# Performance work log

Measured on AMD Instinct MI355X. Metric: run time of the kernel, lower is better.

Reference implementation:

```python
import jax, jax.numpy as jnp
import numpy as np

B, S, D, H = 2, 2048, 1024, 16
HD = D // H  # head_dim = 64


def setup_inputs() -> dict:
    rng = jax.random.key(0)
    ks = jax.random.split(rng, 14)
    s = 0.02
    return {
        "query": jax.random.normal(ks[0], (B, S, D), jnp.float32),
        "key": jax.random.normal(ks[1], (B, S, D), jnp.float32),
        "value": jax.random.normal(ks[2], (B, S, D), jnp.float32),
        "Wq": jax.random.normal(ks[3], (D, D), jnp.float32) * s,
        "bq": jnp.zeros((D,), jnp.float32),
        "Wk": jax.random.normal(ks[4], (D, D), jnp.float32) * s,
        "bk": jnp.zeros((D,), jnp.float32),
        "Wv": jax.random.normal(ks[5], (D, D), jnp.float32) * s,
        "bv": jnp.zeros((D,), jnp.float32),
        "Wo": jax.random.normal(ks[6], (D, D), jnp.float32) * s,
        "bo": jnp.zeros((D,), jnp.float32),
        "Wa": jax.random.normal(ks[7], (3, D, D), jnp.float32) * s,  # 3 aspect projections
        "ba": jnp.zeros((3, D), jnp.float32),
    }


def reference(query, key, value, Wq, bq, Wk, bk, Wv, bv, Wo, bo, Wa, ba):
    scale = 1.0 / jnp.sqrt(jnp.asarray(HD, query.dtype))
    # projections; split heads -> [B, H, S, HD]
    q = (query @ Wq + bq).reshape(B, S, H, HD).transpose(0, 2, 1, 3)
    k = (key @ Wk + bk).reshape(B, S, H, HD).transpose(0, 2, 1, 3)
    v = (value @ Wv + bv).reshape(B, S, H, HD).transpose(0, 2, 1, 3)
    # main attention (dropout p=0, no masks)
    logits = jnp.einsum('bhqd,bhkd->bhqk', q, k) * scale
    attn_weights = jax.nn.softmax(logits, axis=-1)  # [B, H, S, S]
    ctx = jnp.einsum('bhqk,bhkd->bhqd', attn_weights, v)
    attn_output = ctx.transpose(0, 2, 1, 3).reshape(B, S, D) @ Wo + bo
    # 3 interpretable aspect patterns: each proj applied to query and key,
    # full-dim QK^T scaled by sqrt(head_dim), softmax over keys.
    q_asp = jnp.einsum('bsd,ade->abse', query, Wa) + ba[:, None, None, :]
    k_asp = jnp.einsum('bsd,ade->abse', key, Wa) + ba[:, None, None, :]
    pat_logits = jnp.einsum('abqd,abkd->abqk', q_asp, k_asp) * scale
    patterns = jax.nn.softmax(pat_logits, axis=-1)  # [3, B, S, S]
    return attn_output, attn_weights, patterns
```

## Files before the change

kernel.cpp:

```cpp
#include <hip/hip_runtime.h>

typedef unsigned short u16;
typedef short s16x4 __attribute__((ext_vector_type(4)));
typedef short s16x8 __attribute__((ext_vector_type(8)));
typedef float f32x4 __attribute__((ext_vector_type(4)));

#define DEVFN __device__ __forceinline__

constexpr long AW_OFF  = 4194304;
constexpr long PAT_OFF = AW_OFF + 134217728;

DEVFN u16 f2bf(float x) {
  unsigned u = __builtin_bit_cast(unsigned, x);
  unsigned r = (u + 0x7fffu + ((u >> 16) & 1u)) >> 16;
  return (u16)r;
}

DEVFN void gld16(const u16* g, u16* l) {
  __builtin_amdgcn_global_load_lds(
      (const __attribute__((address_space(1))) unsigned int*)g,
      (__attribute__((address_space(3))) unsigned int*)l, 16, 0, 0);
}

__global__ __launch_bounds__(256) void k_cvt3(const float* __restrict__ a,
                                              const float* __restrict__ b,
                                              const float* __restrict__ c,
                                              u16* __restrict__ out, int n4) {
  int i = blockIdx.x * 256 + threadIdx.x;
  if (i >= n4) return;
  const float* in = (blockIdx.y == 0) ? a : (blockIdx.y == 1) ? b : c;
  float4 v = ((const float4*)in)[i];
  s16x4 o; o[0] = f2bf(v.x); o[1] = f2bf(v.y); o[2] = f2bf(v.z); o[3] = f2bf(v.w);
  ((s16x4*)(out + (long)blockIdx.y * 4194304))[i] = o;
}

__global__ __launch_bounds__(256) void k_pack3(const float* __restrict__ a,
                                               const float* __restrict__ b,
                                               const float* __restrict__ c,
                                               float* __restrict__ out) {
  int i = blockIdx.x * 256 + threadIdx.x;
  const float* in = (i < 1024) ? a : (i < 2048) ? b : c;
  out[i] = in[i & 1023];
}

template <bool IN_F32>
__global__ __launch_bounds__(256) void k_tr(const void* __restrict__ inv,
                                            u16* __restrict__ out,
                                            long ldin, long ldout,
                                            long inz1, long inz2, long outz, int zdiv) {
  __shared__ u16 tile[32][33];
  int z = blockIdx.z;
  long ioff = (long)(z / zdiv) * inz1 + (long)(z % zdiv) * inz2;
  int k0 = blockIdx.y * 32, n0 = blockIdx.x * 32;
  int tx = threadIdx.x, ty = threadIdx.y;
#pragma unroll
  for (int i = 0; i < 4; ++i) {
    long k = k0 + ty + i * 8, n = n0 + tx;
    u16 v;
    if constexpr (IN_F32) v = f2bf(((const float*)inv)[ioff + k * ldin + n]);
    else                  v = ((const u16*)inv)[ioff + k * ldin + n];
    tile[ty + i * 8][tx] = v;
  }
  __syncthreads();
  long ooff = (long)z * outz;
#pragma unroll
  for (int i = 0; i < 4; ++i) {
    long n = n0 + ty + i * 8, k = k0 + tx;
    out[ooff + n * ldout + k] = tile[tx][ty + i * 8];
  }
}

template <typename OutT, int EPI>
__global__ __launch_bounds__(256) void k_gemm_nt(
    const u16* __restrict__ Ap, const u16* __restrict__ Bp, OutT* __restrict__ Cp,
    const float* __restrict__ bias, const float* __restrict__ rinv, float alpha, int K,
    long lda, long ldb, long ldc,
    long saz1, long saz2, long sbz1, long sbz2, long scz1, long scz2,
    long sbias, int zdiv) {
  __shared__ __align__(16) u16 At[128][64];
  __shared__ __align__(16) u16 Bt[128][64];
  const int tid = threadIdx.x, lane = tid & 63, wid = tid >> 6;
  const int wm = wid >> 1, wn = wid & 1;

  const int gx = gridDim.x, gy = gridDim.y;
  int id = (blockIdx.z * gy + blockIdx.y) * gx + blockIdx.x;
  const int nb = gx * gy * (int)gridDim.z;
  if ((nb & 7) == 0) id = (id & 7) * (nb >> 3) + (id >> 3);
  const int bxi = id % gx, byi = (id / gx) % gy, bzi = id / (gx * gy);

  const int z = bzi, z1 = z / zdiv, z2 = z % zdiv;
  const u16* Ab = Ap + (long)z1 * saz1 + (long)z2 * saz2;
  const u16* Bb = Bp + (long)z1 * sbz1 + (long)z2 * sbz2;
  OutT* C = Cp + (long)z1 * scz1 + (long)z2 * scz2;
  const float* bv = bias ? bias + (long)z2 * sbias : nullptr;
  const int row0 = byi * 128, col0 = bxi * 128;
  const int lk = lane & 15, g = lane >> 4;

  f32x4 acc[4][4] = {};

  for (int k0 = 0; k0 < K; k0 += 64) {
#pragma unroll
    for (int it = 0; it < 4; ++it) {
      const int u = it * 256 + tid;
      const int r = u >> 3, p = u & 7;
      const int cg = (p ^ (r & 7)) * 8;
      gld16(Ab + (long)(row0 + r) * lda + (k0 + cg), &At[r][p * 8]);
      gld16(Bb + (long)(col0 + r) * ldb + (k0 + cg), &Bt[r][p * 8]);
    }
    __syncthreads();
#pragma unroll
    for (int kk = 0; kk < 2; ++kk) {
      s16x8 af[4], bf[4];
#pragma unroll
      for (int m = 0; m < 4; ++m)
        af[m] = *(const s16x8*)&At[wm * 64 + m * 16 + lk][((kk * 4 + g) ^ (lk & 7)) * 8];
#pragma unroll
      for (int n = 0; n < 4; ++n)
        bf[n] = *(const s16x8*)&Bt[wn * 64 + n * 16 + lk][((kk * 4 + g) ^ (lk & 7)) * 8];
#pragma unroll
      for (int m = 0; m < 4; ++m)
#pragma unroll
        for (int n = 0; n < 4; ++n)
          acc[m][n] = __builtin_amdgcn_mfma_f32_16x16x32_bf16(af[m], bf[n], acc[m][n], 0, 0, 0);
    }
    __syncthreads();
  }

  const float* rz = (EPI == 1) ? rinv + (long)z * 2048 : nullptr;
#pragma unroll
  for (int m = 0; m < 4; ++m) {
    const int grow = row0 + wm * 64 + m * 16 + g * 4;
#pragma unroll
    for (int r = 0; r < 4; ++r) {
      float iv = 0.0f;
      if constexpr (EPI == 1) iv = rz[grow + r];
#pragma unroll
      for (int n = 0; n < 4; ++n) {
        const int gcol = col0 + wn * 64 + n * 16 + lk;
        float v;
        if constexpr (EPI == 1) v = __expf(alpha * acc[m][n][r]) * iv;
        else                    v = alpha * acc[m][n][r] + (bv ? bv[gcol] : 0.0f);
        if constexpr (sizeof(OutT) == 2) C[(long)(grow + r) * ldc + gcol] = f2bf(v);
        else                             C[(long)(grow + r) * ldc + gcol] = v;
      }
    }
  }
}

__global__ __launch_bounds__(256) void k_flash(
    const u16* __restrict__ qp, const u16* __restrict__ kp, const u16* __restrict__ vt,
    u16* __restrict__ ctx, float* __restrict__ rinv) {
  __shared__ __align__(16) char lds[49152];
  u16* Qt = (u16*)lds;
  u16* Kt = (u16*)(lds + 16384);
  u16* Vl = (u16*)(lds + 32768);
  const int tid = threadIdx.x, lane = tid & 63, wid = tid >> 6;
  const int wk = wid >> 1, wq = wid & 1;

  const int gx = gridDim.x;
  int id = blockIdx.y * gx + blockIdx.x;
  const int nb = gx * (int)gridDim.y;
  if ((nb & 7) == 0) id = (id & 7) * (nb >> 3) + (id >> 3);
  const int bh = id / gx, q0 = (id % gx) * 128;

  const long qkbase = (long)(bh >> 4) * 2097152 + (long)(bh & 15) * 64;
  const long vbase = (long)bh * 131072;
  const int lk = lane & 15, g = lane >> 4;
  const int sp = lane & 7;
  const int sr = lane >> 3;

#pragma unroll
  for (int i = 0; i < 4; ++i) {
    const int rr = (wid * 4 + i) * 8 + sr;
    gld16(qp + qkbase + (long)(q0 + rr) * 1024 + ((sp ^ (rr & 7)) * 8), Qt + rr * 64 + sp * 8);
  }
  __syncthreads();

  s16x8 qf[2][4];
#pragma unroll
  for (int kk = 0; kk < 2; ++kk) {
#pragma unroll
    for (int nq = 0; nq < 4; ++nq)
      qf[kk][nq] = *(const s16x8*)(Qt + (wq * 64 + nq * 16 + lk) * 64 + ((kk * 4 + g) ^ (lk & 7)) * 8);
  }

  f32x4 cacc[4][4] = {};
  float rs[4] = {0.f, 0.f, 0.f, 0.f};

  for (int t = 0; t < 16; ++t) {
    const int kb = t * 128;
#pragma unroll
    for (int i = 0; i < 4; ++i) {
      const int rr = (wid * 4 + i) * 8 + sr;
      gld16(kp + qkbase + (long)(kb + rr) * 1024 + ((sp ^ (rr & 7)) * 8), Kt + rr * 64 + sp * 8);
      const int dd = (wid * 4 + i) * 4 + g;
      const int pv = lane & 15;
      const int cv = (pv & 8) | ((pv ^ dd) & 7);
      gld16(vt + vbase + (long)dd * 2048 + (kb + cv * 8), Vl + dd * 128 + pv * 8);
    }
    __syncthreads();

    f32x4 st[4][4] = {};
#pragma unroll
    for (int kk = 0; kk < 2; ++kk) {
      s16x8 af[4];
#pragma unroll
      for (int mk = 0; mk < 4; ++mk)
        af[mk] = *(const s16x8*)(Kt + (wk * 64 + mk * 16 + lk) * 64 + ((kk * 4 + g) ^ (lk & 7)) * 8);
#pragma unroll
      for (int mk = 0; mk < 4; ++mk)
#pragma unroll
        for (int nq = 0; nq < 4; ++nq)
          st[mk][nq] = __builtin_amdgcn_mfma_f32_16x16x32_bf16(af[mk], qf[kk][nq], st[mk][nq], 0, 0, 0);
    }
#pragma unroll
    for (int mk = 0; mk < 4; ++mk)
#pragma unroll
      for (int nq = 0; nq < 4; ++nq)
#pragma unroll
        for (int j = 0; j < 4; ++j) {
          const float p = __expf(st[mk][nq][j] * 0.125f);
          st[mk][nq][j] = p;
          rs[nq] += p;
        }
#pragma unroll
    for (int ks = 0; ks < 2; ++ks) {
      s16x8 pb[4];
#pragma unroll
      for (int nq = 0; nq < 4; ++nq) {
        s16x8 b;
#pragma unroll
        for (int j = 0; j < 4; ++j) {
          b[j]     = (short)f2bf(st[2 * ks][nq][j]);
          b[4 + j] = (short)f2bf(st[2 * ks + 1][nq][j]);
        }
        pb[nq] = b;
      }
#pragma unroll
      for (int md = 0; md < 4; ++md) {
        const int rowv = md * 16 + lk;
        const int u0 = ks * 4 + (g >> 1);
        const int p0 = wk * 8 + ((u0 ^ (rowv & 7)) & 7);
        const int p2 = wk * 8 + (((u0 + 2) ^ (rowv & 7)) & 7);
        const u16* vb0 = Vl + rowv * 128 + p0 * 8 + (g & 1) * 4;
        const u16* vb2 = Vl + rowv * 128 + p2 * 8 + (g & 1) * 4;
        s16x4 lo = *(const s16x4*)vb0;
        s16x4 hi = *(const s16x4*)vb2;
        s16x8 vf;
        vf[0] = lo[0]; vf[1] = lo[1]; vf[2] = lo[2]; vf[3] = lo[3];
        vf[4] = hi[0]; vf[5] = hi[1]; vf[6] = hi[2]; vf[7] = hi[3];
#pragma unroll
        for (int nq = 0; nq < 4; ++nq)
          cacc[md][nq] = __builtin_amdgcn_mfma_f32_16x16x32_bf16(vf, pb[nq], cacc[md][nq], 0, 0, 0);
      }
    }
    __syncthreads();
  }

#pragma unroll
  for (int nq = 0; nq < 4; ++nq) {
    rs[nq] += __shfl_xor(rs[nq], 16, 64);
    rs[nq] += __shfl_xor(rs[nq], 32, 64);
  }
  float* ctxl = (float*)lds;
  float* rsl  = (float*)(lds + 33024);
  if (wk == 1) {
#pragma unroll
    for (int md = 0; md < 4; ++md)
#pragma unroll
      for (int nq = 0; nq < 4; ++nq)
#pragma unroll
        for (int r = 0; r < 4; ++r)
          ctxl[(md * 16 + g * 4 + r) * 129 + wq * 64 + nq * 16 + lk] = cacc[md][nq][r];
    if (lane < 16)
#pragma unroll
      for (int nq = 0; nq < 4; ++nq) rsl[wq * 64 + nq * 16 + lane] = rs[nq];
  }
  __syncthreads();
  if (wk == 0) {
#pragma unroll
    for (int md = 0; md < 4; ++md)
#pragma unroll
      for (int nq = 0; nq < 4; ++nq)
#pragma unroll
        for (int r = 0; r < 4; ++r) {
          const int idx = (md * 16 + g * 4 + r) * 129 + wq * 64 + nq * 16 + lk;
          ctxl[idx] += cacc[md][nq][r];
        }
    if (lane < 16)
#pragma unroll
      for (int nq = 0; nq < 4; ++nq) {
        const int qi = wq * 64 + nq * 16 + lane;
        const float inv = 1.0f / (rsl[qi] + rs[nq]);
        rsl[qi] = inv;
        rinv[(long)bh * 2048 + q0 + qi] = inv;
      }
  }
  __syncthreads();
  const int qr = tid >> 1, half = tid & 1;
  const float inv = rsl[qr];
  u16* dst = ctx + (long)(bh >> 4) * 2097152 + (long)(q0 + qr) * 1024 + (long)(bh & 15) * 64 + half * 32;
#pragma unroll
  for (int c = 0; c < 4; ++c) {
    s16x8 o;
#pragma unroll
    for (int j = 0; j < 8; ++j) {
      const int d = half * 32 + c * 8 + j;
      o[j] = (short)f2bf(ctxl[d * 129 + qr] * inv);
    }
    ((s16x8*)dst)[c] = o;
  }
}

__global__ __launch_bounds__(256) void k_softmax(float* __restrict__ base) {
  float* p = base + (long)blockIdx.x * 2048;
  const int t = threadIdx.x;
  float4 v0 = ((const float4*)p)[t];
  float4 v1 = ((const float4*)p)[t + 256];
  float m = fmaxf(fmaxf(fmaxf(v0.x, v0.y), fmaxf(v0.z, v0.w)),
                  fmaxf(fmaxf(v1.x, v1.y), fmaxf(v1.z, v1.w)));
#pragma unroll
  for (int i = 32; i >= 1; i >>= 1) m = fmaxf(m, __shfl_xor(m, i, 64));
  __shared__ float sm[4], ss[4];
  if ((t & 63) == 0) sm[t >> 6] = m;
  __syncthreads();
  m = fmaxf(fmaxf(sm[0], sm[1]), fmaxf(sm[2], sm[3]));
  float4 e0, e1;
  e0.x = __expf(v0.x - m); e0.y = __expf(v0.y - m); e0.z = __expf(v0.z - m); e0.w = __expf(v0.w - m);
  e1.x = __expf(v1.x - m); e1.y = __expf(v1.y - m); e1.z = __expf(v1.z - m); e1.w = __expf(v1.w - m);
  float s = (e0.x + e0.y + e0.z + e0.w) + (e1.x + e1.y + e1.z + e1.w);
#pragma unroll
  for (int i = 32; i >= 1; i >>= 1) s += __shfl_xor(s, i, 64);
  if ((t & 63) == 0) ss[t >> 6] = s;
  __syncthreads();
  s = ss[0] + ss[1] + ss[2] + ss[3];
  float inv = 1.0f / s;
  e0.x *= inv; e0.y *= inv; e0.z *= inv; e0.w *= inv;
  e1.x *= inv; e1.y *= inv; e1.z *= inv; e1.w *= inv;
  ((float4*)p)[t] = e0;
  ((float4*)p)[t + 256] = e1;
}

extern "C" void kernel_launch(void* const* d_in, const int* in_sizes, int n_in,
                              void* d_out, int out_size, void* d_ws, size_t ws_size,
                              hipStream_t stream) {
  const float* query = (const float*)d_in[0];
  const float* key   = (const float*)d_in[1];
  const float* value = (const float*)d_in[2];
  const float* Wq = (const float*)d_in[3];
  const float* bq = (const float*)d_in[4];
  const float* Wk = (const float*)d_in[5];
  const float* bk = (const float*)d_in[6];
  const float* Wv = (const float*)d_in[7];
  const float* bv = (const float*)d_in[8];
  const float* Wo = (const float*)d_in[9];
  const float* bo = (const float*)d_in[10];
  const float* Wa = (const float*)d_in[11];
  const float* ba = (const float*)d_in[12];
  float* out = (float*)d_out;
  char* ws = (char*)d_ws;

  u16* qb  = (u16*)(ws + 0);
  u16* Wqt = (u16*)(ws + 25165824);
  u16* Wot = (u16*)(ws + 31457280);
  u16* Wat = (u16*)(ws + 33554432);
  u16* qp  = (u16*)(ws + 39845888);
  u16* kp  = (u16*)(ws + 48234496);
  u16* vp  = (u16*)(ws + 56623104);
  u16* vt  = (u16*)(ws + 65011712);
  u16* ctx = (u16*)(ws + 73400320);
  u16* qa  = (u16*)(ws + 81788928);
  float* rinv  = (float*)(ws + 25165824);
  float* pbias = (float*)(ws + 132120576);

  dim3 b256(256);
  dim3 trb(32, 8);

  k_cvt3<<<dim3(4096, 3), b256, 0, stream>>>(query, key, value, qb, 1048576);
  k_pack3<<<12, b256, 0, stream>>>(bq, bk, bv, pbias);

  k_tr<true><<<dim3(32, 32, 1), trb, 0, stream>>>(Wq, Wqt, 1024, 1024, 0, 0, 0, 1);
  k_tr<true><<<dim3(32, 32, 1), trb, 0, stream>>>(Wk, Wqt + 1048576, 1024, 1024, 0, 0, 0, 1);
  k_tr<true><<<dim3(32, 32, 1), trb, 0, stream>>>(Wv, Wqt + 2097152, 1024, 1024, 0, 0, 0, 1);
  k_tr<true><<<dim3(32, 32, 1), trb, 0, stream>>>(Wo, Wot, 1024, 1024, 0, 0, 0, 1);
  k_tr<true><<<dim3(32, 32, 3), trb, 0, stream>>>(Wa, Wat, 1024, 1024, 0, 1048576, 1048576, 3);

  k_gemm_nt<u16, 0><<<dim3(8, 32, 3), b256, 0, stream>>>(
      qb, Wqt, qp, pbias, nullptr, 1.0f, 1024, 1024, 1024, 1024,
      0, 4194304, 0, 1048576, 0, 4194304, 1024, 3);

  k_gemm_nt<u16, 0><<<dim3(8, 32, 6), b256, 0, stream>>>(
      qb, Wat, qa, ba, nullptr, 1.0f, 1024, 1024, 1024, 1024,
      4194304, 0, 0, 1048576, 12582912, 4194304, 1024, 3);

  k_tr<false><<<dim3(2, 64, 32), trb, 0, stream>>>(
      vp, vt, 1024, 2048, 2097152, 64, 131072, 16);

  k_flash<<<dim3(16, 32), b256, 0, stream>>>(qp, kp, vt, ctx, rinv);

  k_gemm_nt<float, 1><<<dim3(16, 16, 32), b256, 0, stream>>>(
      qp, kp, out + AW_OFF, nullptr, rinv, 0.125f, 64, 1024, 1024, 2048,
      2097152, 64, 2097152, 64, 67108864, 4194304, 0, 16);

  k_gemm_nt<float, 0><<<dim3(16, 16, 6), b256, 0, stream>>>(
      qa, qa + 12582912, out + PAT_OFF, nullptr, nullptr, 0.125f, 1024, 1024, 1024, 2048,
      0, 2097152, 0, 2097152, 0, 4194304, 0, 6);

  k_softmax<<<12288, b256, 0, stream>>>(out + PAT_OFF);

  k_gemm_nt<float, 0><<<dim3(8, 32, 1), b256, 0, stream>>>(
      ctx, Wot, out, bo, nullptr, 1.0f, 1024, 1024, 1024, 1024, 0, 0, 0, 0, 0, 0, 0, 1);
}
```

Measured before the change: 509.5 us.

## Add 256x256-tile double-buffered GEMM and merge weight transposes into one launch

Introduces a 512-thread GEMM with 256x256 output tiles, a double-buffered LDS pipeline using direct global-to-LDS loads, and a block-id swizzle across XCDs. It replaces the 128-tile GEMM for the projection, aspect-projection, pattern-logit and output GEMMs. The five weight transpose launches are folded into a single kernel. Larger tiles raise data reuse per block but cut the block count, so the small output GEMM (64 blocks) may underfill the GPU, and the 128 KB of LDS limits each CU to one block.

```diff
diff --git a/kernel.cpp b/kernel.cpp
--- a/kernel.cpp
+++ b/kernel.cpp
@@ -41,6 +41,34 @@
   int i = blockIdx.x * 256 + threadIdx.x;
   const float* in = (i < 1024) ? a : (i < 2048) ? b : c;
   out[i] = in[i & 1023];
+}
+
+__global__ __launch_bounds__(256) void k_trW(const float* __restrict__ Wq,
+                                             const float* __restrict__ Wk,
+                                             const float* __restrict__ Wv,
+                                             const float* __restrict__ Wo,
+                                             const float* __restrict__ Wa,
+                                             u16* __restrict__ Wqt,
+                                             u16* __restrict__ Wot,
+                                             u16* __restrict__ Wat) {
+  __shared__ u16 tile[32][33];
+  const int z = blockIdx.z;
+  const float* in;
+  u16* outp;
+  if (z == 0)      { in = Wq; outp = Wqt; }
+  else if (z == 1) { in = Wk; outp = Wqt + 1048576; }
+  else if (z == 2) { in = Wv; outp = Wqt + 2097152; }
+  else if (z == 3) { in = Wo; outp = Wot; }
+  else             { in = Wa + (long)(z - 4) * 1048576; outp = Wat + (long)(z - 4) * 1048576; }
+  int k0 = blockIdx.y * 32, n0 = blockIdx.x * 32;
+  int tx = threadIdx.x & 31, ty = threadIdx.x >> 5;
+#pragma unroll
+  for (int i = 0; i < 4; ++i)
+    tile[ty + i * 8][tx] = f2bf(in[(long)(k0 + ty + i * 8) * 1024 + (n0 + tx)]);
+  __syncthreads();
+#pragma unroll
+  for (int i = 0; i < 4; ++i)
+    outp[(long)(n0 + ty + i * 8) * 1024 + (k0 + tx)] = tile[tx][ty + i * 8];
 }
 
 template <bool IN_F32>
@@ -130,6 +158,100 @@
 #pragma unroll
   for (int m = 0; m < 4; ++m) {
     const int grow = row0 + wm * 64 + m * 16 + g * 4;
+#pragma unroll
+    for (int r = 0; r < 4; ++r) {
+      float iv = 0.0f;
+      if constexpr (EPI == 1) iv = rz[grow + r];
+#pragma unroll
+      for (int n = 0; n < 4; ++n) {
+        const int gcol = col0 + wn * 64 + n * 16 + lk;
+        float v;
+        if constexpr (EPI == 1) v = __expf(alpha * acc[m][n][r]) * iv;
+        else                    v = alpha * acc[m][n][r] + (bv ? bv[gcol] : 0.0f);
+        if constexpr (sizeof(OutT) == 2) C[(long)(grow + r) * ldc + gcol] = f2bf(v);
+        else                             C[(long)(grow + r) * ldc + gcol] = v;
+      }
+    }
+  }
+}
+
+template <typename OutT, int EPI>
+__global__ __launch_bounds__(512, 1) void k_gemm8(
+    const u16* __restrict__ Ap, const u16* __restrict__ Bp, OutT* __restrict__ Cp,
+    const float* __restrict__ bias, const float* __restrict__ rinv, float alpha, int K,
+    long lda, long ldb, long ldc,
+    long saz1, long saz2, long sbz1, long sbz2, long scz1, long scz2,
+    long sbias, int zdiv) {
+  extern __shared__ __align__(16) u16 dyn[];
+  u16* At = dyn;
+  u16* Bt = dyn + 32768;
+  const int tid = threadIdx.x, lane = tid & 63, wid = tid >> 6;
+  const int wm = wid >> 2, wn = wid & 3;
+
+  const int gx = gridDim.x, gy = gridDim.y;
+  int id = (blockIdx.z * gy + blockIdx.y) * gx + blockIdx.x;
+  const int nb = gx * gy * (int)gridDim.z;
+  if ((nb & 7) == 0) id = (id & 7) * (nb >> 3) + (id >> 3);
+  const int bxi = id % gx, byi = (id / gx) % gy, bzi = id / (gx * gy);
+
+  const int z = bzi, z1 = z / zdiv, z2 = z % zdiv;
+  const u16* Ab = Ap + (long)z1 * saz1 + (long)z2 * saz2;
+  const u16* Bb = Bp + (long)z1 * sbz1 + (long)z2 * sbz2;
+  OutT* C = Cp + (long)z1 * scz1 + (long)z2 * scz2;
+  const float* bv = bias ? bias + (long)z2 * sbias : nullptr;
+  const int row0 = byi * 256, col0 = bxi * 256;
+  const int lk = lane & 15, g = lane >> 4;
+
+  f32x4 acc[8][4] = {};
+  const int NT = K >> 6;
+
+  auto STAGE = [&](int t, int b) {
+    const int k0 = t << 6;
+#pragma unroll
+    for (int it = 0; it < 4; ++it) {
+      const int u = it * 512 + tid;
+      const int r = u >> 3, p = u & 7;
+      const int cg = (p ^ (r & 7)) * 8;
+      gld16(Ab + (long)(row0 + r) * lda + (k0 + cg), At + b * 16384 + r * 64 + p * 8);
+      gld16(Bb + (long)(col0 + r) * ldb + (k0 + cg), Bt + b * 16384 + r * 64 + p * 8);
+    }
+  };
+
+  STAGE(0, 0);
+  STAGE(1, 1);
+  for (int t = 0; t < NT; ++t) {
+    if (t + 1 < NT) asm volatile("s_waitcnt vmcnt(8)" ::: "memory");
+    else            asm volatile("s_waitcnt vmcnt(0)" ::: "memory");
+    __builtin_amdgcn_sched_barrier(0);
+    __builtin_amdgcn_s_barrier();
+    __builtin_amdgcn_sched_barrier(0);
+    const u16* Ax = At + (t & 1) * 16384;
+    const u16* Bx = Bt + (t & 1) * 16384;
+#pragma unroll
+    for (int kk = 0; kk < 2; ++kk) {
+      s16x8 af[8], bf[4];
+#pragma unroll
+      for (int m = 0; m < 8; ++m)
+        af[m] = *(const s16x8*)(Ax + (wm * 128 + m * 16 + lk) * 64 + ((kk * 4 + g) ^ (lk & 7)) * 8);
+#pragma unroll
+      for (int n = 0; n < 4; ++n)
+        bf[n] = *(const s16x8*)(Bx + (wn * 64 + n * 16 + lk) * 64 + ((kk * 4 + g) ^ (lk & 7)) * 8);
+#pragma unroll
+      for (int m = 0; m < 8; ++m)
+#pragma unroll
+        for (int n = 0; n < 4; ++n)
+          acc[m][n] = __builtin_amdgcn_mfma_f32_16x16x32_bf16(af[m], bf[n], acc[m][n], 0, 0, 0);
+    }
+    __builtin_amdgcn_sched_barrier(0);
+    __builtin_amdgcn_s_barrier();
+    __builtin_amdgcn_sched_barrier(0);
+    if (t + 2 < NT) STAGE(t + 2, t & 1);
+  }
+
+  const float* rz = (EPI == 1) ? rinv + (long)z * 2048 : nullptr;
+#pragma unroll
+  for (int m = 0; m < 8; ++m) {
+    const int grow = row0 + wm * 128 + m * 16 + g * 4;
 #pragma unroll
     for (int r = 0; r < 4; ++r) {
       float iv = 0.0f;
@@ -373,23 +495,24 @@
   float* rinv  = (float*)(ws + 25165824);
   float* pbias = (float*)(ws + 132120576);
 
-  dim3 b256(256);
+  hipFuncSetAttribute((const void*)k_gemm8<u16, 0>,
+                      hipFuncAttributeMaxDynamicSharedMemorySize, 131072);
+  hipFuncSetAttribute((const void*)k_gemm8<float, 0>,
+                      hipFuncAttributeMaxDynamicSharedMemorySize, 131072);
+
+  dim3 b256(256), b512(512);
   dim3 trb(32, 8);
 
   k_cvt3<<<dim3(4096, 3), b256, 0, stream>>>(query, key, value, qb, 1048576);
   k_pack3<<<12, b256, 0, stream>>>(bq, bk, bv, pbias);
 
-  k_tr<true><<<dim3(32, 32, 1), trb, 0, stream>>>(Wq, Wqt, 1024, 1024, 0, 0, 0, 1);
-  k_tr<true><<<dim3(32, 32, 1), trb, 0, stream>>>(Wk, Wqt + 1048576, 1024, 1024, 0, 0, 0, 1);
-  k_tr<true><<<dim3(32, 32, 1), trb, 0, stream>>>(Wv, Wqt + 2097152, 1024, 1024, 0, 0, 0, 1);
-  k_tr<true><<<dim3(32, 32, 1), trb, 0, stream>>>(Wo, Wot, 1024, 1024, 0, 0, 0, 1);
-  k_tr<true><<<dim3(32, 32, 3), trb, 0, stream>>>(Wa, Wat, 1024, 1024, 0, 1048576, 1048576, 3);
-
-  k_gemm_nt<u16, 0><<<dim3(8, 32, 3), b256, 0, stream>>>(
+  k_trW<<<dim3(32, 32, 7), b256, 0, stream>>>(Wq, Wk, Wv, Wo, Wa, Wqt, Wot, Wat);
+
+  k_gemm8<u16, 0><<<dim3(4, 16, 3), b512, 131072, stream>>>(
       qb, Wqt, qp, pbias, nullptr, 1.0f, 1024, 1024, 1024, 1024,
       0, 4194304, 0, 1048576, 0, 4194304, 1024, 3);
 
-  k_gemm_nt<u16, 0><<<dim3(8, 32, 6), b256, 0, stream>>>(
+  k_gemm8<u16, 0><<<dim3(4, 16, 6), b512, 131072, stream>>>(
       qb, Wat, qa, ba, nullptr, 1.0f, 1024, 1024, 1024, 1024,
       4194304, 0, 0, 1048576, 12582912, 4194304, 1024, 3);
 
@@ -402,12 +525,13 @@
       qp, kp, out + AW_OFF, nullptr, rinv, 0.125f, 64, 1024, 1024, 2048,
       2097152, 64, 2097152, 64, 67108864, 4194304, 0, 16);
 
-  k_gemm_nt<float, 0><<<dim3(16, 16, 6), b256, 0, stream>>>(
+  k_gemm8<float, 0><<<dim3(8, 8, 6), b512, 131072, stream>>>(
       qa, qa + 12582912, out + PAT_OFF, nullptr, nullptr, 0.125f, 1024, 1024, 1024, 2048,
       0, 2097152, 0, 2097152, 0, 4194304, 0, 6);
 
   k_softmax<<<12288, b256, 0, stream>>>(out + PAT_OFF);
 
-  k_gemm_nt<float, 0><<<dim3(8, 32, 1), b256, 0, stream>>>(
-      ctx, Wot, out, bo, nullptr, 1.0f, 1024, 1024, 1024, 1024, 0, 0, 0, 0, 0, 0, 0, 1);
-}
+  k_gemm8<float, 0><<<dim3(4, 16, 1), b512, 131072, stream>>>(
+      ctx, Wot, out, bo, nullptr, 1.0f, 1024, 1024, 1024, 1024,
+      0, 0, 0, 0, 0, 0, 0, 1);
+}
```

After: 539.9 us. +6.0%, slower.

## Merge weight transposes, projection GEMMs, and attention/pattern logit GEMMs into combined launches

Applied to the files above, without the earlier changes.

Five weight-transpose launches become one k_trW kernel, and the QKV and aspect projection GEMMs become a single 9-slice k_proj9 launch. The memory-bound attention-weights GEMM (K=64) and the compute-heavy pattern-logit GEMM (K=1024) are interleaved in one k_mix grid, so bandwidth-bound and MFMA-bound tiles share the machine at the same time. The expf-with-scale is also replaced by exp2f with a folded log2e constant. The aim is to cut launch overhead and tail effects, at the cost of per-block branching and a hand-built block schedule.

```diff
diff --git a/kernel.cpp b/kernel.cpp
--- a/kernel.cpp
+++ b/kernel.cpp
@@ -9,6 +9,7 @@
 
 constexpr long AW_OFF  = 4194304;
 constexpr long PAT_OFF = AW_OFF + 134217728;
+constexpr float EXPSC  = 0.18033688011f;
 
 DEVFN u16 f2bf(float x) {
   unsigned u = __builtin_bit_cast(unsigned, x);
@@ -43,6 +44,34 @@
   out[i] = in[i & 1023];
 }
 
+__global__ __launch_bounds__(256) void k_trW(const float* __restrict__ Wq,
+                                             const float* __restrict__ Wk,
+                                             const float* __restrict__ Wv,
+                                             const float* __restrict__ Wo,
+                                             const float* __restrict__ Wa,
+                                             u16* __restrict__ Wqt,
+                                             u16* __restrict__ Wot,
+                                             u16* __restrict__ Wat) {
+  __shared__ u16 tile[32][33];
+  const int z = blockIdx.z;
+  const float* in;
+  u16* outp;
+  if (z == 0)      { in = Wq; outp = Wqt; }
+  else if (z == 1) { in = Wk; outp = Wqt + 1048576; }
+  else if (z == 2) { in = Wv; outp = Wqt + 2097152; }
+  else if (z == 3) { in = Wo; outp = Wot; }
+  else             { in = Wa + (long)(z - 4) * 1048576; outp = Wat + (long)(z - 4) * 1048576; }
+  int k0 = blockIdx.y * 32, n0 = blockIdx.x * 32;
+  int tx = threadIdx.x & 31, ty = threadIdx.x >> 5;
+#pragma unroll
+  for (int i = 0; i < 4; ++i)
+    tile[ty + i * 8][tx] = f2bf(in[(long)(k0 + ty + i * 8) * 1024 + (n0 + tx)]);
+  __syncthreads();
+#pragma unroll
+  for (int i = 0; i < 4; ++i)
+    outp[(long)(n0 + ty + i * 8) * 1024 + (k0 + tx)] = tile[tx][ty + i * 8];
+}
+
 template <bool IN_F32>
 __global__ __launch_bounds__(256) void k_tr(const void* __restrict__ inv,
                                             u16* __restrict__ out,
@@ -70,10 +99,40 @@
   }
 }
 
-template <typename OutT, int EPI>
+#define GEMM_CORE(Ab, Bb, lda, ldb, K)                                              \
+  f32x4 acc[4][4] = {};                                                             \
+  for (int k0 = 0; k0 < (K); k0 += 64) {                                            \
+    _Pragma("unroll")                                                               \
+    for (int it = 0; it < 4; ++it) {                                                \
+      const int u = it * 256 + tid;                                                 \
+      const int r = u >> 3, p = u & 7;                                              \
+      const int cg = (p ^ (r & 7)) * 8;                                             \
+      gld16((Ab) + (long)(row0 + r) * (lda) + (k0 + cg), &At[r][p * 8]);            \
+      gld16((Bb) + (long)(col0 + r) * (ldb) + (k0 + cg), &Bt[r][p * 8]);            \
+    }                                                                               \
+    __syncthreads();                                                                \
+    _Pragma("unroll")                                                               \
+    for (int kk = 0; kk < 2; ++kk) {                                                \
+      s16x8 af[4], bf[4];                                                           \
+      _Pragma("unroll")                                                             \
+      for (int m = 0; m < 4; ++m)                                                   \
+        af[m] = *(const s16x8*)&At[wm * 64 + m * 16 + lk][((kk * 4 + g) ^ (lk & 7)) * 8]; \
+      _Pragma("unroll")                                                             \
+      for (int n = 0; n < 4; ++n)                                                   \
+        bf[n] = *(const s16x8*)&Bt[wn * 64 + n * 16 + lk][((kk * 4 + g) ^ (lk & 7)) * 8]; \
+      _Pragma("unroll")                                                             \
+      for (int m = 0; m < 4; ++m)                                                   \
+        _Pragma("unroll")                                                           \
+        for (int n = 0; n < 4; ++n)                                                 \
+          acc[m][n] = __builtin_amdgcn_mfma_f32_16x16x32_bf16(af[m], bf[n], acc[m][n], 0, 0, 0); \
+    }                                                                               \
+    __syncthreads();                                                                \
+  }
+
+template <typename OutT>
 __global__ __launch_bounds__(256) void k_gemm_nt(
     const u16* __restrict__ Ap, const u16* __restrict__ Bp, OutT* __restrict__ Cp,
-    const float* __restrict__ bias, const float* __restrict__ rinv, float alpha, int K,
+    const float* __restrict__ bias, float alpha, int K,
     long lda, long ldb, long ldc,
     long saz1, long saz2, long sbz1, long sbz2, long scz1, long scz2,
     long sbias, int zdiv) {
@@ -96,52 +155,120 @@
   const int row0 = byi * 128, col0 = bxi * 128;
   const int lk = lane & 15, g = lane >> 4;
 
-  f32x4 acc[4][4] = {};
-
-  for (int k0 = 0; k0 < K; k0 += 64) {
-#pragma unroll
-    for (int it = 0; it < 4; ++it) {
-      const int u = it * 256 + tid;
-      const int r = u >> 3, p = u & 7;
-      const int cg = (p ^ (r & 7)) * 8;
-      gld16(Ab + (long)(row0 + r) * lda + (k0 + cg), &At[r][p * 8]);
-      gld16(Bb + (long)(col0 + r) * ldb + (k0 + cg), &Bt[r][p * 8]);
-    }
-    __syncthreads();
-#pragma unroll
-    for (int kk = 0; kk < 2; ++kk) {
-      s16x8 af[4], bf[4];
-#pragma unroll
-      for (int m = 0; m < 4; ++m)
-        af[m] = *(const s16x8*)&At[wm * 64 + m * 16 + lk][((kk * 4 + g) ^ (lk & 7)) * 8];
-#pragma unroll
-      for (int n = 0; n < 4; ++n)
-        bf[n] = *(const s16x8*)&Bt[wn * 64 + n * 16 + lk][((kk * 4 + g) ^ (lk & 7)) * 8];
-#pragma unroll
-      for (int m = 0; m < 4; ++m)
-#pragma unroll
-        for (int n = 0; n < 4; ++n)
-          acc[m][n] = __builtin_amdgcn_mfma_f32_16x16x32_bf16(af[m], bf[n], acc[m][n], 0, 0, 0);
-    }
-    __syncthreads();
-  }
-
-  const float* rz = (EPI == 1) ? rinv + (long)z * 2048 : nullptr;
+  GEMM_CORE(Ab, Bb, lda, ldb, K)
+
 #pragma unroll
   for (int m = 0; m < 4; ++m) {
     const int grow = row0 + wm * 64 + m * 16 + g * 4;
 #pragma unroll
     for (int r = 0; r < 4; ++r) {
-      float iv = 0.0f;
-      if constexpr (EPI == 1) iv = rz[grow + r];
+#pragma unroll
+      for (int n = 0; n < 4; ++n) {
+        const int gcol = col0 + wn * 64 + n * 16 + lk;
+        float v = alpha * acc[m][n][r] + (bv ? bv[gcol] : 0.0f);
+        if constexpr (sizeof(OutT) == 2) C[(long)(grow + r) * ldc + gcol] = f2bf(v);
+        else                             C[(long)(grow + r) * ldc + gcol] = v;
+      }
+    }
+  }
+}
+
+__global__ __launch_bounds__(256) void k_proj9(
+    const u16* __restrict__ qb, const u16* __restrict__ Wqt, const u16* __restrict__ Wat,
+    u16* __restrict__ qp, u16* __restrict__ qa,
+    const float* __restrict__ pbias, const float* __restrict__ ba) {
+  __shared__ __align__(16) u16 At[128][64];
+  __shared__ __align__(16) u16 Bt[128][64];
+  const int tid = threadIdx.x, lane = tid & 63, wid = tid >> 6;
+  const int wm = wid >> 1, wn = wid & 1;
+
+  const int gx = gridDim.x, gy = gridDim.y;
+  int id = (blockIdx.z * gy + blockIdx.y) * gx + blockIdx.x;
+  const int nb = gx * gy * (int)gridDim.z;
+  id = (id & 7) * (nb >> 3) + (id >> 3);
+  const int bxi = id % gx, byi = (id / gx) % gy, z = id / (gx * gy);
+
+  const u16 *Ab, *Bb;
+  u16* C;
+  const float* bv;
+  if (z < 3) {
+    Ab = qb + (long)z * 4194304; Bb = Wqt + (long)z * 1048576;
+    C = qp + (long)z * 4194304;  bv = pbias + (long)z * 1024;
+  } else {
+    const int z1 = (z - 3) / 3, z2 = (z - 3) % 3;
+    Ab = qb + (long)z1 * 4194304; Bb = Wat + (long)z2 * 1048576;
+    C = qa + (long)z1 * 12582912 + (long)z2 * 4194304; bv = ba + (long)z2 * 1024;
+  }
+  const int row0 = byi * 128, col0 = bxi * 128;
+  const int lk = lane & 15, g = lane >> 4;
+
+  GEMM_CORE(Ab, Bb, 1024, 1024, 1024)
+
+#pragma unroll
+  for (int m = 0; m < 4; ++m) {
+    const int grow = row0 + wm * 64 + m * 16 + g * 4;
+#pragma unroll
+    for (int r = 0; r < 4; ++r) {
+#pragma unroll
+      for (int n = 0; n < 4; ++n) {
+        const int gcol = col0 + wn * 64 + n * 16 + lk;
+        C[(long)(grow + r) * 1024 + gcol] = f2bf(acc[m][n][r] + bv[gcol]);
+      }
+    }
+  }
+}
+
+__global__ __launch_bounds__(256) void k_mix(
+    const u16* __restrict__ qp, const u16* __restrict__ kp,
+    const u16* __restrict__ qa, const u16* __restrict__ ka,
+    float* __restrict__ aw, float* __restrict__ pat,
+    const float* __restrict__ rinv) {
+  __shared__ __align__(16) u16 At[128][64];
+  __shared__ __align__(16) u16 Bt[128][64];
+  const int tid = threadIdx.x, lane = tid & 63, wid = tid >> 6;
+  const int wm = wid >> 1, wn = wid & 1;
+  const int lk = lane & 15, g = lane >> 4;
+
+  const int id = blockIdx.x;
+  const int cx = id & 7, pos = id >> 3;
+  const int grp = pos / 19, r19 = pos % 19;
+  const bool isw = (r19 < 16);
+  int z, by, bx, K;
+  const u16 *Ab, *Bb;
+  float* C;
+  if (isw) {
+    const int w = cx * 1024 + grp * 16 + r19;
+    z = w >> 8; const int t = w & 255; by = t >> 4; bx = t & 15;
+    Ab = qp + (long)(z >> 4) * 2097152 + (long)(z & 15) * 64;
+    Bb = kp + (long)(z >> 4) * 2097152 + (long)(z & 15) * 64;
+    C  = aw + (long)z * 4194304;
+    K = 64;
+  } else {
+    const int p = cx * 192 + grp * 3 + (r19 - 16);
+    z = p >> 8; const int t = p & 255; by = t >> 4; bx = t & 15;
+    Ab = qa + (long)z * 2097152;
+    Bb = ka + (long)z * 2097152;
+    C  = pat + (long)z * 4194304;
+    K = 1024;
+  }
+  const int row0 = by * 128, col0 = bx * 128;
+
+  GEMM_CORE(Ab, Bb, 1024, 1024, K)
+
+  const float* rz = rinv + (long)z * 2048;
+#pragma unroll
+  for (int m = 0; m < 4; ++m) {
+    const int grow = row0 + wm * 64 + m * 16 + g * 4;
+#pragma unroll
+    for (int r = 0; r < 4; ++r) {
+      const float iv = isw ? rz[grow + r] : 0.0f;
 #pragma unroll
       for (int n = 0; n < 4; ++n) {
         const int gcol = col0 + wn * 64 + n * 16 + lk;
         float v;
-        if constexpr (EPI == 1) v = __expf(alpha * acc[m][n][r]) * iv;
-        else                    v = alpha * acc[m][n][r] + (bv ? bv[gcol] : 0.0f);
-        if constexpr (sizeof(OutT) == 2) C[(long)(grow + r) * ldc + gcol] = f2bf(v);
-        else                             C[(long)(grow + r) * ldc + gcol] = v;
+        if (isw) v = exp2f(acc[m][n][r] * EXPSC) * iv;
+        else     v = 0.125f * acc[m][n][r];
+        C[(long)(grow + r) * 2048 + gcol] = v;
       }
     }
   }
@@ -219,7 +346,7 @@
       for (int nq = 0; nq < 4; ++nq)
 #pragma unroll
         for (int j = 0; j < 4; ++j) {
-          const float p = __expf(st[mk][nq][j] * 0.125f);
+          const float p = exp2f(st[mk][nq][j] * EXPSC);
           st[mk][nq][j] = p;
           rs[nq] += p;
         }
@@ -379,35 +506,20 @@
   k_cvt3<<<dim3(4096, 3), b256, 0, stream>>>(query, key, value, qb, 1048576);
   k_pack3<<<12, b256, 0, stream>>>(bq, bk, bv, pbias);
 
-  k_tr<true><<<dim3(32, 32, 1), trb, 0, stream>>>(Wq, Wqt, 1024, 1024, 0, 0, 0, 1);
-  k_tr<true><<<dim3(32, 32, 1), trb, 0, stream>>>(Wk, Wqt + 1048576, 1024, 1024, 0, 0, 0, 1);
-  k_tr<true><<<dim3(32, 32, 1), trb, 0, stream>>>(Wv, Wqt + 2097152, 1024, 1024, 0, 0, 0, 1);
-  k_tr<true><<<dim3(32, 32, 1), trb, 0, stream>>>(Wo, Wot, 1024, 1024, 0, 0, 0, 1);
-  k_tr<true><<<dim3(32, 32, 3), trb, 0, stream>>>(Wa, Wat, 1024, 1024, 0, 1048576, 1048576, 3);
-
-  k_gemm_nt<u16, 0><<<dim3(8, 32, 3), b256, 0, stream>>>(
-      qb, Wqt, qp, pbias, nullptr, 1.0f, 1024, 1024, 1024, 1024,
-      0, 4194304, 0, 1048576, 0, 4194304, 1024, 3);
-
-  k_gemm_nt<u16, 0><<<dim3(8, 32, 6), b256, 0, stream>>>(
-      qb, Wat, qa, ba, nullptr, 1.0f, 1024, 1024, 1024, 1024,
-      4194304, 0, 0, 1048576, 12582912, 4194304, 1024, 3);
+  k_trW<<<dim3(32, 32, 7), b256, 0, stream>>>(Wq, Wk, Wv, Wo, Wa, Wqt, Wot, Wat);
+
+  k_proj9<<<dim3(8, 32, 9), b256, 0, stream>>>(qb, Wqt, Wat, qp, qa, pbias, ba);
 
   k_tr<false><<<dim3(2, 64, 32), trb, 0, stream>>>(
       vp, vt, 1024, 2048, 2097152, 64, 131072, 16);
 
   k_flash<<<dim3(16, 32), b256, 0, stream>>>(qp, kp, vt, ctx, rinv);
 
-  k_gemm_nt<float, 1><<<dim3(16, 16, 32), b256, 0, stream>>>(
-      qp, kp, out + AW_OFF, nullptr, rinv, 0.125f, 64, 1024, 1024, 2048,
-      2097152, 64, 2097152, 64, 67108864, 4194304, 0, 16);
-
-  k_gemm_nt<float, 0><<<dim3(16, 16, 6), b256, 0, stream>>>(
-      qa, qa + 12582912, out + PAT_OFF, nullptr, nullptr, 0.125f, 1024, 1024, 1024, 2048,
-      0, 2097152, 0, 2097152, 0, 4194304, 0, 6);
+  k_mix<<<9728, b256, 0, stream>>>(qp, kp, qa, qa + 12582912,
+                                   out + AW_OFF, out + PAT_OFF, rinv);
 
   k_softmax<<<12288, b256, 0, stream>>>(out + PAT_OFF);
 
-  k_gemm_nt<float, 0><<<dim3(8, 32, 1), b256, 0, stream>>>(
-      ctx, Wot, out, bo, nullptr, 1.0f, 1024, 1024, 1024, 1024, 0, 0, 0, 0, 0, 0, 0, 1);
-}
+  k_gemm_nt<float><<<dim3(8, 32, 1), b256, 0, stream>>>(
+      ctx, Wot, out, bo, 1.0f, 1024, 1024, 1024, 1024, 0, 0, 0, 0, 0, 0, 0, 1);
+}
```

New measurement: 569.3 us. +11.7%, slower.
